# Kernel tuning notes

Measured on AMD Instinct MI355X. Metric: run time of the kernel, lower is better.

## Reference

```python
import jax, jax.numpy as jnp
import numpy as np

H, W, T = 128, 128, 4
BLOCK_W = 16
N = 1024
CHOL_BOUND = jnp.array([0.5, 0.0, 0.0, 0.5, 0.0, 0.5], dtype=jnp.float32)  # diag lower bound
SCALE = 2.0 * BLOCK_W / W  # gaussian footprint ~ tile-sized in normalized [-1,1] coords


def setup_inputs() -> dict:
    key = jax.random.key(0)
    k1, k2, k3, k4 = jax.random.split(key, 4)
    return {
        "xyz_3D": jax.random.normal(k1, (N, 3), dtype=jnp.float32),
        "cholesky_3D": jax.random.uniform(k2, (N, 6), dtype=jnp.float32),
        "features_dc_3D": jax.random.uniform(k3, (N, 3), dtype=jnp.float32),
        "opacity_3D": jax.random.normal(k4, (N, 1), dtype=jnp.float32),
    }


def _splat(xyz, chol6, feats, opac):
    # activations (match module properties)
    means = jnp.tanh(xyz)                      # [N,3] in [-1,1], (x,y,t)
    c = chol6 + CHOL_BOUND[None, :]            # [N,6]
    alpha_g = jax.nn.sigmoid(opac)             # [N,1]

    # lower-triangular L: rows (x,y,t); layout (0,0)=c0,(1,0)=c1,(2,0)=c2,(1,1)=c3,(2,1)=c4,(2,2)=c5
    zeros = jnp.zeros_like(c[:, 0])
    L = jnp.stack([
        jnp.stack([c[:, 0], zeros,   zeros], -1),
        jnp.stack([c[:, 1], c[:, 3], zeros], -1),
        jnp.stack([c[:, 2], c[:, 4], c[:, 5]], -1),
    ], axis=1) * SCALE                          # [N,3,3]
    Sigma = jnp.einsum('nij,nkj->nik', L, L)    # L L^T, [N,3,3]
    Sinv = jnp.linalg.inv(Sigma)                # [N,3,3]

    # voxel-center grids in normalized [-1,1]
    xs = (jnp.arange(W, dtype=jnp.float32) + 0.5) / W * 2.0 - 1.0
    ys = (jnp.arange(H, dtype=jnp.float32) + 0.5) / H * 2.0 - 1.0
    ts = (jnp.arange(T, dtype=jnp.float32) + 0.5) / T * 2.0 - 1.0

    dx = xs[None, :] - means[:, 0:1]            # [N,W]
    dy = ys[None, :] - means[:, 1:2]            # [N,H]
    dt = ts[None, :] - means[:, 2:3]            # [N,T]

    a  = Sinv[:, 0, 0][:, None, None, None]
    b  = Sinv[:, 1, 1][:, None, None, None]
    cc = Sinv[:, 2, 2][:, None, None, None]
    ab = Sinv[:, 0, 1][:, None, None, None]
    at = Sinv[:, 0, 2][:, None, None, None]
    bt = Sinv[:, 1, 2][:, None, None, None]

    dxw = dx[:, None, None, :]                  # [N,1,1,W]
    dyh = dy[:, None, :, None]                  # [N,1,H,1]
    dtt = dt[:, :, None, None]                  # [N,T,1,1]

    # quadratic form d^T Sigma^{-1} d over the full [N,T,H,W] grid
    q = (a * dxw * dxw + b * dyh * dyh + cc * dtt * dtt
         + 2.0 * ab * dxw * dyh + 2.0 * at * dxw * dtt + 2.0 * bt * dyh * dtt)

    dens = alpha_g[:, :, None, None] * jnp.exp(-0.5 * q)   # [N,T,H,W]
    img = jnp.einsum('nthw,nc->thwc', dens, feats)          # [T,H,W,3]
    return jnp.clip(img, 0.0, 1.0)


def reference(xyz_3D, cholesky_3D, features_dc_3D, opacity_3D):
    return _splat(xyz_3D, cholesky_3D, features_dc_3D, opacity_3D)
```

## Files before the change

kernel.cpp:

```cpp
#include <hip/hip_runtime.h>
#include <hip/hip_fp16.h>


#define GV_H 128
#define GV_W 128
#define GV_T 4
#define GV_NMAX 1024
#define GV_DX 0.015625f
#define K_HALF_LOG2E (-0.72134752044448170f)
#define GV_LOG2E 1.44269504088896340f
#define U_CULL (-20.0f)

typedef float f32x2 __attribute__((ext_vector_type(2)));

__device__ __forceinline__ float fexp2(float x) { return __builtin_amdgcn_exp2f(x); }
__device__ __forceinline__ float frcp(float x)  { return __builtin_amdgcn_rcpf(x); }
__device__ __forceinline__ float flog2(float x) { return __builtin_amdgcn_logf(x); }

__device__ __forceinline__ float fast_tanh(float x) {
    float t = fexp2(2.885390082f * x);
    return fmaf(-2.0f, frcp(t + 1.0f), 1.0f);
}

__global__ __launch_bounds__(512, 3) void gv_fused_kernel(
    const float* __restrict__ xyz, const float* __restrict__ chol,
    const float* __restrict__ feats, const float* __restrict__ opac,
    float* __restrict__ out, int N)
{
    __shared__ __align__(16) float stab[GV_NMAX * 8];
    __shared__ int swt[16];

    int b    = blockIdx.x;
    int xq   = b & 3;
    int slab = (b >> 2) & 63;
    int t    = b >> 8;
    int tid  = threadIdx.x;
    int wv   = tid >> 6;
    int lane = tid & 63;

    float y0r = ((float)(slab * 2) + 0.5f) * GV_DX - 1.0f;
    float y1r = y0r + GV_DX;
    float xlo = ((float)(xq * 32) + 0.5f) * GV_DX - 1.0f;
    float xhi = xlo + 31.0f * GV_DX;

    float4 rec0[2], rec1[2];
    bool keep[2];
    unsigned long long bm[2];

    #pragma unroll
    for (int r = 0; r < 2; ++r) {
        keep[r] = false;
        rec0[r] = make_float4(0.f, 0.f, -1e30f, -1e30f);
        rec1[r] = make_float4(0.f, 0.f, 0.f, 0.f);
        int n = r * 512 + tid;
        if (n < N) {
            float mx = fast_tanh(xyz[n * 3 + 0]);
            float my = fast_tanh(xyz[n * 3 + 1]);
            float mt = fast_tanh(xyz[n * 3 + 2]);

            const float sc = 2.0f * 16.0f / (float)GV_W;
            float L00 = sc * (chol[n * 6 + 0] + 0.5f);
            float L10 = sc * (chol[n * 6 + 1]);
            float L20 = sc * (chol[n * 6 + 2]);
            float L11 = sc * (chol[n * 6 + 3] + 0.5f);
            float L21 = sc * (chol[n * 6 + 4]);
            float L22 = sc * (chol[n * 6 + 5] + 0.5f);

            float il0 = frcp(L00), il1 = frcp(L11), il2 = frcp(L22);
            float m10 = -L10 * il0 * il1;
            float m21 = -L21 * il1 * il2;
            float m20 = (L10 * L21 - L11 * L20) * (il0 * il1 * il2);
            float a   = il0 * il0 + m10 * m10 + m20 * m20;
            float sab = m10 * il1 + m20 * m21;
            float sat = m20 * il2;
            float bb  = il1 * il1 + m21 * m21;
            float sbt = m21 * il2;
            float cc  = il2 * il2;
            float ab2 = 2.0f * sab, at2 = 2.0f * sat, bt2 = 2.0f * sbt;

            float o = opac[n];
            float bias = -flog2(1.0f + fexp2(-GV_LOG2E * o));

            float tv = ((float)t + 0.5f) * (2.0f / (float)GV_T) - 1.0f;
            float dt = tv - mt;

            const float k = K_HALF_LOG2E;
            float A  = k * a;
            float B  = k * bb;
            float C  = k * ab2;
            float Dx = k * (at2 * dt - 2.0f * a * mx - ab2 * my);
            float Dy = k * (bt2 * dt - 2.0f * bb * my - ab2 * mx);
            float E  = k * (a * mx * mx + bb * my * my + cc * dt * dt
                            + ab2 * mx * my - at2 * mx * dt - bt2 * my * dt)
                       + bias;

            float gy0 = fmaf(C, y0r, Dx);
            float gy1 = fmaf(C, y1r, Dx);
            float h0  = fmaf(fmaf(B, y0r, Dy), y0r, E);
            float h1  = fmaf(fmaf(B, y1r, Dy), y1r, E);
            float ss  = fexp2(A * (8.0f * GV_DX * GV_DX));

            float fr = feats[n * 3 + 0];
            float fg = feats[n * 3 + 1];
            float fb = feats[n * 3 + 2];
            unsigned hr = (unsigned)__half_as_ushort(__float2half_rn(fr))
                        | ((unsigned)__half_as_ushort(__float2half_rn(fg)) << 16);
            float rgbits = __uint_as_float(hr);

            float inv2A = 0.5f * frcp(A);
            float xs0 = fminf(fmaxf(-gy0 * inv2A, xlo), xhi);
            float xs1 = fminf(fmaxf(-gy1 * inv2A, xlo), xhi);
            float u0  = fmaf(fmaf(A, xs0, gy0), xs0, h0);
            float u1  = fmaf(fmaf(A, xs1, gy1), xs1, h1);
            keep[r] = (fmaxf(u0, u1) > U_CULL);

            rec0[r] = make_float4(gy0, gy1, h0, h1);
            rec1[r] = make_float4(A, ss, rgbits, fb);
        }
        bm[r] = __ballot((int)keep[r]);
    }

    if (lane == 0) {
        swt[wv]     = (int)__popcll(bm[0]);
        swt[8 + wv] = (int)__popcll(bm[1]);
    }
    __syncthreads();

    int M = 0, base0 = 0, base1 = 0;
    #pragma unroll
    for (int k2 = 0; k2 < 16; ++k2) {
        int c = swt[k2];
        if (k2 < wv)     base0 += c;
        if (k2 < 8 + wv) base1 += c;
        M += c;
    }
    unsigned long long lmask = (1ull << lane) - 1ull;
    if (keep[0]) {
        float4* dst = (float4*)&stab[(base0 + (int)__popcll(bm[0] & lmask)) * 8];
        dst[0] = rec0[0]; dst[1] = rec1[0];
    }
    if (keep[1]) {
        float4* dst = (float4*)&stab[(base1 + (int)__popcll(bm[1] & lmask)) * 8];
        dst[0] = rec0[1]; dst[1] = rec1[1];
    }
    int MP = (M + 63) & ~63;
    #pragma unroll
    for (int r = 0; r < 2; ++r) {
        int di = r * 512 + tid;
        if (di >= M && di < MP) {
            float4* dst = (float4*)&stab[di * 8];
            dst[0] = make_float4(0.f, 0.f, -1e30f, -1e30f);
            dst[1] = make_float4(0.f, 0.f, 0.f, 0.f);
        }
    }
    __syncthreads();

    int slot = lane >> 3;
    int pg   = lane & 7;
    int oct  = pg & 3;
    int row  = pg >> 2;

    float x0  = ((float)(xq * 32 + oct * 8) + 0.5f) * GV_DX - 1.0f;
    float caa = 2.0f * x0 + GV_DX;
    const float c2d2 = 2.0f * GV_DX * GV_DX;
    bool r1 = (row == 1);

    f32x2 aR[4], aG[4], aB[4];
    #pragma unroll
    for (int j = 0; j < 4; ++j) {
        aR[j] = (f32x2)(0.f); aG[j] = (f32x2)(0.f); aB[j] = (f32x2)(0.f);
    }

    int iters = MP >> 6;
    const float4* rp = (const float4*)&stab[(wv * 8 + slot) * 8];

    #pragma unroll 1
    for (int it = 0; it < iters; ++it) {
        float4 q0 = rp[0];
        float4 q1 = rp[1];
        rp += 64 * 2;

        float gy = r1 ? q0.y : q0.x;
        float h  = r1 ? q0.w : q0.z;
        float A  = q1.x;

        float u0 = fmaf(fmaf(A, x0, gy), x0, h);
        float d0 = GV_DX * fmaf(A, caa, gy);
        float t1 = A * c2d2;
        float p0 = fmaf(2.0f, d0, t1);
        float p1 = fmaf(2.0f, t1, p0);

        f32x2 e2  = { fexp2(u0), fexp2(u0 + d0) };
        f32x2 rr2 = { fexp2(p0), fexp2(p1) };
        f32x2 ss2 = { q1.y, q1.y };

        unsigned bits = __float_as_uint(q1.z);
        float fr = __half2float(__ushort_as_half((unsigned short)(bits & 0xffffu)));
        float fg = __half2float(__ushort_as_half((unsigned short)(bits >> 16)));
        f32x2 fr2 = { fr, fr };
        f32x2 fg2 = { fg, fg };
        f32x2 fb2 = { q1.w, q1.w };

        #pragma unroll
        for (int j = 0; j < 4; ++j) {
            aR[j] = __builtin_elementwise_fma(e2, fr2, aR[j]);
            aG[j] = __builtin_elementwise_fma(e2, fg2, aG[j]);
            aB[j] = __builtin_elementwise_fma(e2, fb2, aB[j]);
            if (j < 3) { e2 *= rr2; rr2 *= ss2; }
        }
    }

    #pragma unroll
    for (int j = 0; j < 4; ++j) {
        #pragma unroll
        for (int m = 8; m <= 32; m <<= 1) {
            aR[j][0] += __shfl_xor(aR[j][0], m, 64);
            aR[j][1] += __shfl_xor(aR[j][1], m, 64);
            aG[j][0] += __shfl_xor(aG[j][0], m, 64);
            aG[j][1] += __shfl_xor(aG[j][1], m, 64);
            aB[j][0] += __shfl_xor(aB[j][0], m, 64);
            aB[j][1] += __shfl_xor(aB[j][1], m, 64);
        }
    }

    __syncthreads();

    if (slot == 0) {
        float* dst = &stab[wv * 208 + pg * 26];
        #pragma unroll
        for (int j = 0; j < 4; ++j) {
            dst[j * 6 + 0] = aR[j][0];
            dst[j * 6 + 1] = aR[j][1];
            dst[j * 6 + 2] = aG[j][0];
            dst[j * 6 + 3] = aG[j][1];
            dst[j * 6 + 4] = aB[j][0];
            dst[j * 6 + 5] = aB[j][1];
        }
    }
    __syncthreads();

    if (tid < 192) {
        int c   = tid % 3;
        int px  = tid / 3;
        int x   = px & 31;
        int rw  = px >> 5;
        int oc  = x >> 3;
        int p8  = x & 7;
        int j   = p8 >> 1;
        int cmp = p8 & 1;
        int ofs = (rw * 4 + oc) * 26 + j * 6 + c * 2 + cmp;
        float sum = 0.f;
        #pragma unroll
        for (int w = 0; w < 8; ++w) sum += stab[w * 208 + ofs];
        int idx = ((t * GV_H + slab * 2 + rw) * GV_W + xq * 32 + x) * 3 + c;
        out[idx] = fminf(fmaxf(sum, 0.0f), 1.0f);
    }
}

extern "C" void kernel_launch(void* const* d_in, const int* in_sizes, int n_in,
                              void* d_out, int out_size, void* d_ws, size_t ws_size,
                              hipStream_t stream) {
    const float* xyz   = (const float*)d_in[0];
    const float* chol  = (const float*)d_in[1];
    const float* feats = (const float*)d_in[2];
    const float* opac  = (const float*)d_in[3];
    float* out = (float*)d_out;
    int N = in_sizes[0] / 3;
    if (N > GV_NMAX) N = GV_NMAX;

    int blocks = GV_T * 64 * 4;
    gv_fused_kernel<<<blocks, 512, 0, stream>>>(xyz, chol, feats, opac, out, N);
}
```

Before: 21.15 us.

## Assign one full image row per block with two gaussians per iteration

Changes the block decomposition from 2-row by 32-column tiles to one full 128-pixel row per block, halving the block count. This halves the redundant per-block gaussian preprocessing. Each lane now covers 8 pixels and processes two gaussians per loop iteration for more ILP, and the compacted record shrinks to six floats. The cost is weaker culling: the x extent is the whole image, so more gaussians survive per block and the inner-loop work per pixel grows.

```diff
diff --git a/kernel.cpp b/kernel.cpp
--- a/kernel.cpp
+++ b/kernel.cpp
@@ -31,27 +31,24 @@
     __shared__ int swt[16];
 
     int b    = blockIdx.x;
-    int xq   = b & 3;
-    int slab = (b >> 2) & 63;
-    int t    = b >> 8;
+    int slab = b & 127;
+    int t    = b >> 7;
     int tid  = threadIdx.x;
     int wv   = tid >> 6;
     int lane = tid & 63;
 
-    float y0r = ((float)(slab * 2) + 0.5f) * GV_DX - 1.0f;
-    float y1r = y0r + GV_DX;
-    float xlo = ((float)(xq * 32) + 0.5f) * GV_DX - 1.0f;
-    float xhi = xlo + 31.0f * GV_DX;
-
-    float4 rec0[2], rec1[2];
+    float yr = ((float)slab + 0.5f) * GV_DX - 1.0f;
+
+    float4 rec0[2];
+    float2 rec1[2];
     bool keep[2];
     unsigned long long bm[2];
 
     #pragma unroll
     for (int r = 0; r < 2; ++r) {
         keep[r] = false;
-        rec0[r] = make_float4(0.f, 0.f, -1e30f, -1e30f);
-        rec1[r] = make_float4(0.f, 0.f, 0.f, 0.f);
+        rec0[r] = make_float4(0.f, -1e30f, 0.f, 0.f);
+        rec1[r] = make_float2(0.f, 0.f);
         int n = r * 512 + tid;
         if (n < N) {
             float mx = fast_tanh(xyz[n * 3 + 0]);
@@ -94,28 +91,23 @@
                             + ab2 * mx * my - at2 * mx * dt - bt2 * my * dt)
                        + bias;
 
-            float gy0 = fmaf(C, y0r, Dx);
-            float gy1 = fmaf(C, y1r, Dx);
-            float h0  = fmaf(fmaf(B, y0r, Dy), y0r, E);
-            float h1  = fmaf(fmaf(B, y1r, Dy), y1r, E);
-            float ss  = fexp2(A * (8.0f * GV_DX * GV_DX));
+            float gy = fmaf(C, yr, Dx);
+            float h  = fmaf(fmaf(B, yr, Dy), yr, E);
+            float ss = fexp2(A * (8.0f * GV_DX * GV_DX));
 
             float fr = feats[n * 3 + 0];
             float fg = feats[n * 3 + 1];
             float fb = feats[n * 3 + 2];
             unsigned hr = (unsigned)__half_as_ushort(__float2half_rn(fr))
                         | ((unsigned)__half_as_ushort(__float2half_rn(fg)) << 16);
-            float rgbits = __uint_as_float(hr);
 
             float inv2A = 0.5f * frcp(A);
-            float xs0 = fminf(fmaxf(-gy0 * inv2A, xlo), xhi);
-            float xs1 = fminf(fmaxf(-gy1 * inv2A, xlo), xhi);
-            float u0  = fmaf(fmaf(A, xs0, gy0), xs0, h0);
-            float u1  = fmaf(fmaf(A, xs1, gy1), xs1, h1);
-            keep[r] = (fmaxf(u0, u1) > U_CULL);
-
-            rec0[r] = make_float4(gy0, gy1, h0, h1);
-            rec1[r] = make_float4(A, ss, rgbits, fb);
+            float xs = fminf(fmaxf(-gy * inv2A, -1.0f), 1.0f);
+            float u  = fmaf(fmaf(A, xs, gy), xs, h);
+            keep[r] = (u > U_CULL);
+
+            rec0[r] = make_float4(gy, h, A, ss);
+            rec1[r] = make_float2(__uint_as_float(hr), fb);
         }
         bm[r] = __ballot((int)keep[r]);
     }
@@ -136,34 +128,32 @@
     }
     unsigned long long lmask = (1ull << lane) - 1ull;
     if (keep[0]) {
-        float4* dst = (float4*)&stab[(base0 + (int)__popcll(bm[0] & lmask)) * 8];
-        dst[0] = rec0[0]; dst[1] = rec1[0];
+        int di = base0 + (int)__popcll(bm[0] & lmask);
+        *(float4*)&stab[di * 8]     = rec0[0];
+        *(float2*)&stab[di * 8 + 4] = rec1[0];
     }
     if (keep[1]) {
-        float4* dst = (float4*)&stab[(base1 + (int)__popcll(bm[1] & lmask)) * 8];
-        dst[0] = rec0[1]; dst[1] = rec1[1];
+        int di = base1 + (int)__popcll(bm[1] & lmask);
+        *(float4*)&stab[di * 8]     = rec0[1];
+        *(float2*)&stab[di * 8 + 4] = rec1[1];
     }
     int MP = (M + 63) & ~63;
     #pragma unroll
     for (int r = 0; r < 2; ++r) {
         int di = r * 512 + tid;
         if (di >= M && di < MP) {
-            float4* dst = (float4*)&stab[di * 8];
-            dst[0] = make_float4(0.f, 0.f, -1e30f, -1e30f);
-            dst[1] = make_float4(0.f, 0.f, 0.f, 0.f);
-        }
-    }
-    __syncthreads();
-
-    int slot = lane >> 3;
-    int pg   = lane & 7;
-    int oct  = pg & 3;
-    int row  = pg >> 2;
-
-    float x0  = ((float)(xq * 32 + oct * 8) + 0.5f) * GV_DX - 1.0f;
+            *(float4*)&stab[di * 8]     = make_float4(0.f, -1e30f, 0.f, 0.f);
+            *(float2*)&stab[di * 8 + 4] = make_float2(0.f, 0.f);
+        }
+    }
+    __syncthreads();
+
+    int slot = lane >> 4;
+    int li   = lane & 15;
+
+    float x0  = ((float)(li * 8) + 0.5f) * GV_DX - 1.0f;
     float caa = 2.0f * x0 + GV_DX;
     const float c2d2 = 2.0f * GV_DX * GV_DX;
-    bool r1 = (row == 1);
 
     f32x2 aR[4], aG[4], aB[4];
     #pragma unroll
@@ -172,48 +162,63 @@
     }
 
     int iters = MP >> 6;
-    const float4* rp = (const float4*)&stab[(wv * 8 + slot) * 8];
+    const float* rp = &stab[(wv * 8 + slot * 2) * 8];
 
     #pragma unroll 1
     for (int it = 0; it < iters; ++it) {
-        float4 q0 = rp[0];
-        float4 q1 = rp[1];
-        rp += 64 * 2;
-
-        float gy = r1 ? q0.y : q0.x;
-        float h  = r1 ? q0.w : q0.z;
-        float A  = q1.x;
-
-        float u0 = fmaf(fmaf(A, x0, gy), x0, h);
-        float d0 = GV_DX * fmaf(A, caa, gy);
-        float t1 = A * c2d2;
-        float p0 = fmaf(2.0f, d0, t1);
-        float p1 = fmaf(2.0f, t1, p0);
-
-        f32x2 e2  = { fexp2(u0), fexp2(u0 + d0) };
-        f32x2 rr2 = { fexp2(p0), fexp2(p1) };
-        f32x2 ss2 = { q1.y, q1.y };
-
-        unsigned bits = __float_as_uint(q1.z);
-        float fr = __half2float(__ushort_as_half((unsigned short)(bits & 0xffffu)));
-        float fg = __half2float(__ushort_as_half((unsigned short)(bits >> 16)));
-        f32x2 fr2 = { fr, fr };
-        f32x2 fg2 = { fg, fg };
-        f32x2 fb2 = { q1.w, q1.w };
+        float4 qa0 = *(const float4*)(rp);
+        float2 qa1 = *(const float2*)(rp + 4);
+        float4 qb0 = *(const float4*)(rp + 8);
+        float2 qb1 = *(const float2*)(rp + 12);
+        rp += 64 * 8;
+
+        float u0a = fmaf(fmaf(qa0.z, x0, qa0.x), x0, qa0.y);
+        float d0a = GV_DX * fmaf(qa0.z, caa, qa0.x);
+        float t1a = qa0.z * c2d2;
+        float p0a = fmaf(2.0f, d0a, t1a);
+        float p1a = fmaf(2.0f, t1a, p0a);
+        f32x2 ea2  = { fexp2(u0a), fexp2(u0a + d0a) };
+        f32x2 rra2 = { fexp2(p0a), fexp2(p1a) };
+        f32x2 ssa2 = { qa0.w, qa0.w };
+        unsigned bia = __float_as_uint(qa1.x);
+        float fra = __half2float(__ushort_as_half((unsigned short)(bia & 0xffffu)));
+        float fga = __half2float(__ushort_as_half((unsigned short)(bia >> 16)));
+        f32x2 fra2 = { fra, fra }, fga2 = { fga, fga };
+        f32x2 fba2 = { qa1.y, qa1.y };
+
+        float u0b = fmaf(fmaf(qb0.z, x0, qb0.x), x0, qb0.y);
+        float d0b = GV_DX * fmaf(qb0.z, caa, qb0.x);
+        float t1b = qb0.z * c2d2;
+        float p0b = fmaf(2.0f, d0b, t1b);
+        float p1b = fmaf(2.0f, t1b, p0b);
+        f32x2 eb2  = { fexp2(u0b), fexp2(u0b + d0b) };
+        f32x2 rrb2 = { fexp2(p0b), fexp2(p1b) };
+        f32x2 ssb2 = { qb0.w, qb0.w };
+        unsigned bib = __float_as_uint(qb1.x);
+        float frb = __half2float(__ushort_as_half((unsigned short)(bib & 0xffffu)));
+        float fgb = __half2float(__ushort_as_half((unsigned short)(bib >> 16)));
+        f32x2 frb2 = { frb, frb }, fgb2 = { fgb, fgb };
+        f32x2 fbb2 = { qb1.y, qb1.y };
 
         #pragma unroll
         for (int j = 0; j < 4; ++j) {
-            aR[j] = __builtin_elementwise_fma(e2, fr2, aR[j]);
-            aG[j] = __builtin_elementwise_fma(e2, fg2, aG[j]);
-            aB[j] = __builtin_elementwise_fma(e2, fb2, aB[j]);
-            if (j < 3) { e2 *= rr2; rr2 *= ss2; }
+            aR[j] = __builtin_elementwise_fma(ea2, fra2, aR[j]);
+            aG[j] = __builtin_elementwise_fma(ea2, fga2, aG[j]);
+            aB[j] = __builtin_elementwise_fma(ea2, fba2, aB[j]);
+            aR[j] = __builtin_elementwise_fma(eb2, frb2, aR[j]);
+            aG[j] = __builtin_elementwise_fma(eb2, fgb2, aG[j]);
+            aB[j] = __builtin_elementwise_fma(eb2, fbb2, aB[j]);
+            if (j < 3) {
+                ea2 *= rra2; rra2 *= ssa2;
+                eb2 *= rrb2; rrb2 *= ssb2;
+            }
         }
     }
 
     #pragma unroll
     for (int j = 0; j < 4; ++j) {
         #pragma unroll
-        for (int m = 8; m <= 32; m <<= 1) {
+        for (int m = 16; m <= 32; m <<= 1) {
             aR[j][0] += __shfl_xor(aR[j][0], m, 64);
             aR[j][1] += __shfl_xor(aR[j][1], m, 64);
             aG[j][0] += __shfl_xor(aG[j][0], m, 64);
@@ -226,7 +231,7 @@
     __syncthreads();
 
     if (slot == 0) {
-        float* dst = &stab[wv * 208 + pg * 26];
+        float* dst = &stab[wv * 400 + li * 25];
         #pragma unroll
         for (int j = 0; j < 4; ++j) {
             dst[j * 6 + 0] = aR[j][0];
@@ -239,20 +244,18 @@
     }
     __syncthreads();
 
-    if (tid < 192) {
+    if (tid < GV_W * 3) {
         int c   = tid % 3;
         int px  = tid / 3;
-        int x   = px & 31;
-        int rw  = px >> 5;
-        int oc  = x >> 3;
-        int p8  = x & 7;
+        int li2 = px >> 3;
+        int p8  = px & 7;
         int j   = p8 >> 1;
         int cmp = p8 & 1;
-        int ofs = (rw * 4 + oc) * 26 + j * 6 + c * 2 + cmp;
+        int ofs = li2 * 25 + j * 6 + c * 2 + cmp;
         float sum = 0.f;
         #pragma unroll
-        for (int w = 0; w < 8; ++w) sum += stab[w * 208 + ofs];
-        int idx = ((t * GV_H + slab * 2 + rw) * GV_W + xq * 32 + x) * 3 + c;
+        for (int w = 0; w < 8; ++w) sum += stab[w * 400 + ofs];
+        int idx = ((t * GV_H + slab) * GV_W + px) * 3 + c;
         out[idx] = fminf(fmaxf(sum, 0.0f), 1.0f);
     }
 }
@@ -268,6 +271,6 @@
     int N = in_sizes[0] / 3;
     if (N > GV_NMAX) N = GV_NMAX;
 
-    int blocks = GV_T * 64 * 4;
+    int blocks = GV_T * GV_H;
     gv_fused_kernel<<<blocks, 512, 0, stream>>>(xyz, chol, feats, opac, out, N);
 }
```

Result: faster. 18.71 us (-11.5%).
